# Kernel optimization log

Measured on AMD Instinct MI355X. Metric: run time of the kernel, lower is better.

The kernel has to match this reference:

```python
import jax, jax.numpy as jnp
import numpy as np

B, C, H, W_sp = 32, 64, 64, 64
K, D = 512, 64

def setup_inputs() -> dict:
    key = jax.random.key(0)
    k1, k2 = jax.random.split(key)
    x = jax.random.normal(k1, (B, C, H, W_sp), dtype=jnp.float32)
    # codebook init uniform(-1/K, 1/K) as in the torch module
    W = jax.random.uniform(k2, (K, D), dtype=jnp.float32, minval=-1.0 / K, maxval=1.0 / K)
    return {"x": x, "W": W}

def reference(x, W):
    # NCHW -> NHWC, flatten to [N, D]
    inputs = jnp.transpose(x, (0, 2, 3, 1))  # [B,H,W,D]
    input_shape = inputs.shape
    flat = inputs.reshape(-1, D)  # [N, D]
    # squared euclidean distances [N, K]
    distances = (jnp.sum(flat * flat, axis=1, keepdims=True)
                 + jnp.sum(W * W, axis=1)
                 - 2.0 * jnp.matmul(flat, W.T))
    encoding_indices = jnp.argmin(distances, axis=1)[:, None]  # [N,1]
    encodings = jax.nn.one_hot(encoding_indices[:, 0], K, dtype=jnp.float32)  # [N,K]
    # direct gather instead of one-hot matmul (same math)
    quantized = W[encoding_indices[:, 0]].reshape(input_shape)  # [B,H,W,D]
    # straight-through estimator
    quantized = inputs + jax.lax.stop_gradient(quantized - inputs)
    avg_probs = jnp.mean(encodings, axis=0)  # [K]
    perplexity = jnp.exp(-jnp.sum(avg_probs * jnp.log(avg_probs + 1e-10)))
    quantized = jnp.transpose(quantized, (0, 3, 1, 2))  # back to NCHW
    return (distances, encodings, encoding_indices, quantized, perplexity)
```

## Files before the change

kernel.cpp:

```cpp
#include <hip/hip_runtime.h>
#include <float.h>
#include <math.h>

#define NROWS 131072
#define KCB   512
#define DDIM  64
#define HWSP  4096
#define BCHW  8388608

__global__ __launch_bounds__(256) void vq_main(const float* __restrict__ x,
                                               const float* __restrict__ Wc,
                                               float* __restrict__ dist,
                                               float* __restrict__ enc,
                                               float* __restrict__ idxo) {
    __shared__ float lx[DDIM][64];
    __shared__ float lw[DDIM][68];
    __shared__ float lxsq[64];
    __shared__ float lwsq[64];

    const int t  = threadIdx.x;
    const int n0 = blockIdx.x * 64;
    const int b  = n0 >> 12;
    const int s0 = n0 & (HWSP - 1);

    {
        const int s = t & 63, cq = t >> 6;
        const float* xb = x + (size_t)b * DDIM * HWSP + s0 + s;
#pragma unroll
        for (int it = 0; it < 16; ++it) {
            const int c = it * 4 + cq;
            lx[c][s] = xb[(size_t)c * HWSP];
        }
    }
    __syncthreads();
    if (t < 64) {
        float s = 0.f;
#pragma unroll
        for (int d = 0; d < DDIM; ++d) { const float v = lx[d][t]; s += v * v; }
        lxsq[t] = s;
    }

    const int rg = t >> 4;
    const int kg = t & 15;

    float best[4] = {FLT_MAX, FLT_MAX, FLT_MAX, FLT_MAX};
    int   bidx[4] = {0, 0, 0, 0};

    for (int kt = 0; kt < 8; ++kt) {
        __syncthreads();
        {
            const int d = t & 63, kq0 = t >> 6;
            const float* wb = Wc + (size_t)(kt * 64) * DDIM + d;
#pragma unroll
            for (int it = 0; it < 16; ++it) {
                const int kq = it * 4 + kq0;
                lw[d][kq] = wb[(size_t)kq * DDIM];
            }
        }
        __syncthreads();
        if (t < 64) {
            float s = 0.f;
#pragma unroll
            for (int d = 0; d < DDIM; ++d) { const float w = lw[d][t]; s += w * w; }
            lwsq[t] = s;
        }
        __syncthreads();

        float acc[4][4] = {};
#pragma unroll 4
        for (int d = 0; d < DDIM; ++d) {
            const float4 xv = *(const float4*)&lx[d][rg * 4];
            const float4 wv = *(const float4*)&lw[d][kg * 4];
            acc[0][0] += xv.x * wv.x; acc[0][1] += xv.x * wv.y; acc[0][2] += xv.x * wv.z; acc[0][3] += xv.x * wv.w;
            acc[1][0] += xv.y * wv.x; acc[1][1] += xv.y * wv.y; acc[1][2] += xv.y * wv.z; acc[1][3] += xv.y * wv.w;
            acc[2][0] += xv.z * wv.x; acc[2][1] += xv.z * wv.y; acc[2][2] += xv.z * wv.z; acc[2][3] += xv.z * wv.w;
            acc[3][0] += xv.w * wv.x; acc[3][1] += xv.w * wv.y; acc[3][2] += xv.w * wv.z; acc[3][3] += xv.w * wv.w;
        }

        const int kbase = kt * 64 + kg * 4;
        const float4 wq = *(const float4*)&lwsq[kg * 4];
        const float4 z4 = make_float4(0.f, 0.f, 0.f, 0.f);
#pragma unroll
        for (int r = 0; r < 4; ++r) {
            const int n = n0 + rg * 4 + r;
            const float xs = lxsq[rg * 4 + r];
            float4 dv;
            dv.x = xs + wq.x - 2.f * acc[r][0];
            dv.y = xs + wq.y - 2.f * acc[r][1];
            dv.z = xs + wq.z - 2.f * acc[r][2];
            dv.w = xs + wq.w - 2.f * acc[r][3];
            *(float4*)&dist[(size_t)n * KCB + kbase] = dv;
            *(float4*)&enc [(size_t)n * KCB + kbase] = z4;
            const float dd[4] = {dv.x, dv.y, dv.z, dv.w};
#pragma unroll
            for (int j = 0; j < 4; ++j) {
                const int kk = kbase + j;
                if (dd[j] < best[r] || (dd[j] == best[r] && kk < bidx[r])) {
                    best[r] = dd[j]; bidx[r] = kk;
                }
            }
        }
    }

#pragma unroll
    for (int off = 8; off >= 1; off >>= 1) {
#pragma unroll
        for (int r = 0; r < 4; ++r) {
            const float od = __shfl_xor(best[r], off);
            const int   oi = __shfl_xor(bidx[r], off);
            if (od < best[r] || (od == best[r] && oi < bidx[r])) { best[r] = od; bidx[r] = oi; }
        }
    }

    __syncthreads();
    if (kg == 0) {
#pragma unroll
        for (int r = 0; r < 4; ++r) {
            const int n = n0 + rg * 4 + r;
            idxo[n] = (float)bidx[r];
            enc[(size_t)n * KCB + bidx[r]] = 1.0f;
        }
    }
}

__global__ __launch_bounds__(256) void vq_quant(const float* __restrict__ Wc,
                                                const float* __restrict__ idxf,
                                                float* __restrict__ qout) {
    __shared__ float lq[64][65];
    __shared__ int   codes[64];

    const int t  = threadIdx.x;
    const int n0 = blockIdx.x * 64;
    const int b  = n0 >> 12;
    const int s0 = n0 & (HWSP - 1);

    if (t < 64) codes[t] = (int)idxf[n0 + t];
    __syncthreads();
    {
        const int c = t & 63, rq = t >> 6;
#pragma unroll
        for (int it = 0; it < 16; ++it) {
            const int r = it * 4 + rq;
            lq[r][c] = Wc[(size_t)codes[r] * DDIM + c];
        }
    }
    __syncthreads();
    {
        const int s = t & 63, cq = t >> 6;
        float* qb = qout + (size_t)b * DDIM * HWSP + s0 + s;
#pragma unroll
        for (int it = 0; it < 16; ++it) {
            const int c = it * 4 + cq;
            qb[(size_t)c * HWSP] = lq[s][c];
        }
    }
}

__global__ __launch_bounds__(512) void vq_perp(const float* __restrict__ idxf,
                                               float* __restrict__ perp) {
    __shared__ unsigned int lh[KCB];
    __shared__ float red[8];
    const int t = threadIdx.x;
    lh[t] = 0u;
    __syncthreads();
    for (int i = t; i < NROWS; i += 512)
        atomicAdd(&lh[(int)idxf[i]], 1u);
    __syncthreads();
    const float p = (float)lh[t] * (1.0f / (float)NROWS);
    float term = p * logf(p + 1e-10f);
#pragma unroll
    for (int off = 32; off >= 1; off >>= 1) term += __shfl_down(term, off);
    if ((t & 63) == 0) red[t >> 6] = term;
    __syncthreads();
    if (t == 0) {
        float s = 0.f;
#pragma unroll
        for (int i = 0; i < 8; ++i) s += red[i];
        *perp = expf(-s);
    }
}

extern "C" void kernel_launch(void* const* d_in, const int* in_sizes, int n_in,
                              void* d_out, int out_size, void* d_ws, size_t ws_size,
                              hipStream_t stream) {
    const float* x  = (const float*)d_in[0];
    const float* Wc = (const float*)d_in[1];

    float* out = (float*)d_out;
    const size_t NK = (size_t)NROWS * KCB;
    float* dist  = out;
    float* enc   = out + NK;
    float* idxo  = out + 2 * NK;
    float* quant = idxo + NROWS;
    float* perp  = quant + (size_t)BCHW;

    (void)d_ws; (void)ws_size;

    vq_main <<<NROWS / 64, 256, 0, stream>>>(x, Wc, dist, enc, idxo);
    vq_quant<<<NROWS / 64, 256, 0, stream>>>(Wc, idxo, quant);
    vq_perp <<<1,          512, 0, stream>>>(idxo, perp);
}
```

Baseline: 717.8 us.

## Enlarge distance-GEMM register tile to 8x8 and precompute codebook norms once

The main kernel now processes 128 rows per block against 128-code tiles. Each thread holds an 8x8 accumulator instead of 4x4, which gives more FMAs per shared-memory load and halves the number of codebook reloads per row. All 512 codebook squared norms are computed once per block from global memory rather than per tile, which removes one barrier per tile. The perplexity histogram kernel moves to 1024 threads with float4 index loads. The larger accumulator raises register pressure and may reduce occupancy, while the kernel remains dominated by the large distance and one-hot output writes.

```diff
diff --git a/kernel.cpp b/kernel.cpp
--- a/kernel.cpp
+++ b/kernel.cpp
@@ -8,117 +8,148 @@
 #define HWSP  4096
 #define BCHW  8388608
 
+#define BM    128
+#define BKT   128
+#define NT    4
+
 __global__ __launch_bounds__(256) void vq_main(const float* __restrict__ x,
                                                const float* __restrict__ Wc,
                                                float* __restrict__ dist,
                                                float* __restrict__ enc,
                                                float* __restrict__ idxo) {
-    __shared__ float lx[DDIM][64];
-    __shared__ float lw[DDIM][68];
-    __shared__ float lxsq[64];
-    __shared__ float lwsq[64];
+    __shared__ float lx[DDIM][BM];
+    __shared__ float lw[DDIM][BKT];
+    __shared__ float lxsq[BM];
+    __shared__ float lwsq[KCB];
 
     const int t  = threadIdx.x;
-    const int n0 = blockIdx.x * 64;
+    const int n0 = blockIdx.x * BM;
     const int b  = n0 >> 12;
     const int s0 = n0 & (HWSP - 1);
 
     {
-        const int s = t & 63, cq = t >> 6;
-        const float* xb = x + (size_t)b * DDIM * HWSP + s0 + s;
-#pragma unroll
-        for (int it = 0; it < 16; ++it) {
-            const int c = it * 4 + cq;
+        const int s = t & 127, cq = t >> 7;
+        const float* xb = x + (size_t)b * (DDIM * HWSP) + s0 + s;
+#pragma unroll
+        for (int it = 0; it < 32; ++it) {
+            const int c = it * 2 + cq;
             lx[c][s] = xb[(size_t)c * HWSP];
         }
     }
-    __syncthreads();
-    if (t < 64) {
+    {
+#pragma unroll
+        for (int kk = 0; kk < 2; ++kk) {
+            const int k = t + kk * 256;
+            const float4* wr = (const float4*)(Wc + (size_t)k * DDIM);
+            float s = 0.f;
+#pragma unroll
+            for (int j = 0; j < 16; ++j) {
+                const float4 v = wr[j];
+                s += v.x * v.x + v.y * v.y + v.z * v.z + v.w * v.w;
+            }
+            lwsq[k] = s;
+        }
+    }
+    __syncthreads();
+    if (t < BM) {
         float s = 0.f;
 #pragma unroll
         for (int d = 0; d < DDIM; ++d) { const float v = lx[d][t]; s += v * v; }
         lxsq[t] = s;
     }
 
-    const int rg = t >> 4;
-    const int kg = t & 15;
-
-    float best[4] = {FLT_MAX, FLT_MAX, FLT_MAX, FLT_MAX};
-    int   bidx[4] = {0, 0, 0, 0};
-
-    for (int kt = 0; kt < 8; ++kt) {
+    const int tr = t >> 4;
+    const int tc = t & 15;
+
+    float best[8];
+    int   bidx[8];
+#pragma unroll
+    for (int i = 0; i < 8; ++i) { best[i] = FLT_MAX; bidx[i] = 0; }
+
+    for (int kt = 0; kt < NT; ++kt) {
         __syncthreads();
         {
             const int d = t & 63, kq0 = t >> 6;
-            const float* wb = Wc + (size_t)(kt * 64) * DDIM + d;
-#pragma unroll
-            for (int it = 0; it < 16; ++it) {
+            const float* wb = Wc + (size_t)(kt * BKT) * DDIM + d;
+#pragma unroll
+            for (int it = 0; it < 32; ++it) {
                 const int kq = it * 4 + kq0;
                 lw[d][kq] = wb[(size_t)kq * DDIM];
             }
         }
         __syncthreads();
-        if (t < 64) {
-            float s = 0.f;
-#pragma unroll
-            for (int d = 0; d < DDIM; ++d) { const float w = lw[d][t]; s += w * w; }
-            lwsq[t] = s;
-        }
-        __syncthreads();
-
-        float acc[4][4] = {};
+
+        float acc[8][8] = {};
 #pragma unroll 4
         for (int d = 0; d < DDIM; ++d) {
-            const float4 xv = *(const float4*)&lx[d][rg * 4];
-            const float4 wv = *(const float4*)&lw[d][kg * 4];
-            acc[0][0] += xv.x * wv.x; acc[0][1] += xv.x * wv.y; acc[0][2] += xv.x * wv.z; acc[0][3] += xv.x * wv.w;
-            acc[1][0] += xv.y * wv.x; acc[1][1] += xv.y * wv.y; acc[1][2] += xv.y * wv.z; acc[1][3] += xv.y * wv.w;
-            acc[2][0] += xv.z * wv.x; acc[2][1] += xv.z * wv.y; acc[2][2] += xv.z * wv.z; acc[2][3] += xv.z * wv.w;
-            acc[3][0] += xv.w * wv.x; acc[3][1] += xv.w * wv.y; acc[3][2] += xv.w * wv.z; acc[3][3] += xv.w * wv.w;
-        }
-
-        const int kbase = kt * 64 + kg * 4;
-        const float4 wq = *(const float4*)&lwsq[kg * 4];
+            const float4 xv0 = *(const float4*)&lx[d][tr * 4];
+            const float4 xv1 = *(const float4*)&lx[d][64 + tr * 4];
+            const float4 wv0 = *(const float4*)&lw[d][tc * 4];
+            const float4 wv1 = *(const float4*)&lw[d][64 + tc * 4];
+            const float xv[8] = {xv0.x, xv0.y, xv0.z, xv0.w, xv1.x, xv1.y, xv1.z, xv1.w};
+            const float wv[8] = {wv0.x, wv0.y, wv0.z, wv0.w, wv1.x, wv1.y, wv1.z, wv1.w};
+#pragma unroll
+            for (int i = 0; i < 8; ++i)
+#pragma unroll
+                for (int j = 0; j < 8; ++j)
+                    acc[i][j] += xv[i] * wv[j];
+        }
+
+        const int kb = kt * BKT;
         const float4 z4 = make_float4(0.f, 0.f, 0.f, 0.f);
 #pragma unroll
-        for (int r = 0; r < 4; ++r) {
-            const int n = n0 + rg * 4 + r;
-            const float xs = lxsq[rg * 4 + r];
-            float4 dv;
-            dv.x = xs + wq.x - 2.f * acc[r][0];
-            dv.y = xs + wq.y - 2.f * acc[r][1];
-            dv.z = xs + wq.z - 2.f * acc[r][2];
-            dv.w = xs + wq.w - 2.f * acc[r][3];
-            *(float4*)&dist[(size_t)n * KCB + kbase] = dv;
-            *(float4*)&enc [(size_t)n * KCB + kbase] = z4;
-            const float dd[4] = {dv.x, dv.y, dv.z, dv.w};
-#pragma unroll
-            for (int j = 0; j < 4; ++j) {
-                const int kk = kbase + j;
-                if (dd[j] < best[r] || (dd[j] == best[r] && kk < bidx[r])) {
-                    best[r] = dd[j]; bidx[r] = kk;
+        for (int h = 0; h < 2; ++h)
+#pragma unroll
+        for (int i = 0; i < 4; ++i) {
+            const int r = h * 64 + tr * 4 + i;
+            const int n = n0 + r;
+            const float xs = lxsq[r];
+            float* drow = &dist[(size_t)n * KCB + kb];
+            float* erow = &enc [(size_t)n * KCB + kb];
+#pragma unroll
+            for (int g = 0; g < 2; ++g) {
+                const int kc = g * 64 + tc * 4;
+                const float4 wq = *(const float4*)&lwsq[kb + kc];
+                float4 dv;
+                dv.x = xs + wq.x - 2.f * acc[h * 4 + i][g * 4 + 0];
+                dv.y = xs + wq.y - 2.f * acc[h * 4 + i][g * 4 + 1];
+                dv.z = xs + wq.z - 2.f * acc[h * 4 + i][g * 4 + 2];
+                dv.w = xs + wq.w - 2.f * acc[h * 4 + i][g * 4 + 3];
+                *(float4*)&drow[kc] = dv;
+                *(float4*)&erow[kc] = z4;
+                const float dd[4] = {dv.x, dv.y, dv.z, dv.w};
+#pragma unroll
+                for (int j = 0; j < 4; ++j) {
+                    const int kk = kb + kc + j;
+                    const int a  = h * 4 + i;
+                    if (dd[j] < best[a] || (dd[j] == best[a] && kk < bidx[a])) {
+                        best[a] = dd[j]; bidx[a] = kk;
+                    }
                 }
             }
         }
     }
 
 #pragma unroll
-    for (int off = 8; off >= 1; off >>= 1) {
-#pragma unroll
-        for (int r = 0; r < 4; ++r) {
-            const float od = __shfl_xor(best[r], off);
-            const int   oi = __shfl_xor(bidx[r], off);
-            if (od < best[r] || (od == best[r] && oi < bidx[r])) { best[r] = od; bidx[r] = oi; }
-        }
-    }
-
-    __syncthreads();
-    if (kg == 0) {
-#pragma unroll
-        for (int r = 0; r < 4; ++r) {
-            const int n = n0 + rg * 4 + r;
-            idxo[n] = (float)bidx[r];
-            enc[(size_t)n * KCB + bidx[r]] = 1.0f;
+    for (int off = 8; off >= 1; off >>= 1)
+#pragma unroll
+        for (int i = 0; i < 8; ++i) {
+            const float od = __shfl_xor(best[i], off);
+            const int   oi = __shfl_xor(bidx[i], off);
+            if (od < best[i] || (od == best[i] && oi < bidx[i])) { best[i] = od; bidx[i] = oi; }
+        }
+
+    __syncthreads();
+    if (tc == 0) {
+#pragma unroll
+        for (int h = 0; h < 2; ++h)
+#pragma unroll
+        for (int i = 0; i < 4; ++i) {
+            const int r  = h * 64 + tr * 4 + i;
+            const int n  = n0 + r;
+            const int bi = bidx[h * 4 + i];
+            idxo[n] = (float)bi;
+            enc[(size_t)n * KCB + bi] = 1.0f;
         }
     }
 }
@@ -147,7 +178,7 @@
     __syncthreads();
     {
         const int s = t & 63, cq = t >> 6;
-        float* qb = qout + (size_t)b * DDIM * HWSP + s0 + s;
+        float* qb = qout + (size_t)b * (DDIM * HWSP) + s0 + s;
 #pragma unroll
         for (int it = 0; it < 16; ++it) {
             const int c = it * 4 + cq;
@@ -156,18 +187,29 @@
     }
 }
 
-__global__ __launch_bounds__(512) void vq_perp(const float* __restrict__ idxf,
-                                               float* __restrict__ perp) {
+__global__ __launch_bounds__(1024) void vq_perp(const float* __restrict__ idxf,
+                                                float* __restrict__ perp) {
     __shared__ unsigned int lh[KCB];
-    __shared__ float red[8];
+    __shared__ float red[16];
     const int t = threadIdx.x;
-    lh[t] = 0u;
-    __syncthreads();
-    for (int i = t; i < NROWS; i += 512)
-        atomicAdd(&lh[(int)idxf[i]], 1u);
-    __syncthreads();
-    const float p = (float)lh[t] * (1.0f / (float)NROWS);
-    float term = p * logf(p + 1e-10f);
+    if (t < KCB) lh[t] = 0u;
+    if (t < 16) red[t] = 0.f;
+    __syncthreads();
+    const float4* p4 = (const float4*)idxf;
+#pragma unroll 4
+    for (int j = 0; j < 32; ++j) {
+        const float4 v = p4[t + j * 1024];
+        atomicAdd(&lh[(int)v.x], 1u);
+        atomicAdd(&lh[(int)v.y], 1u);
+        atomicAdd(&lh[(int)v.z], 1u);
+        atomicAdd(&lh[(int)v.w], 1u);
+    }
+    __syncthreads();
+    float term = 0.f;
+    if (t < KCB) {
+        const float p = (float)lh[t] * (1.0f / (float)NROWS);
+        term = p * logf(p + 1e-10f);
+    }
 #pragma unroll
     for (int off = 32; off >= 1; off >>= 1) term += __shfl_down(term, off);
     if ((t & 63) == 0) red[t >> 6] = term;
@@ -175,7 +217,7 @@
     if (t == 0) {
         float s = 0.f;
 #pragma unroll
-        for (int i = 0; i < 8; ++i) s += red[i];
+        for (int i = 0; i < 16; ++i) s += red[i];
         *perp = expf(-s);
     }
 }
@@ -196,7 +238,7 @@
 
     (void)d_ws; (void)ws_size;
 
-    vq_main <<<NROWS / 64, 256, 0, stream>>>(x, Wc, dist, enc, idxo);
-    vq_quant<<<NROWS / 64, 256, 0, stream>>>(Wc, idxo, quant);
-    vq_perp <<<1,          512, 0, stream>>>(idxo, perp);
-}
+    vq_main <<<NROWS / BM, 256,  0, stream>>>(x, Wc, dist, enc, idxo);
+    vq_quant<<<NROWS / 64, 256,  0, stream>>>(Wc, idxo, quant);
+    vq_perp <<<1,          1024, 0, stream>>>(idxo, perp);
+}
```

Result: slower. 736.3 us (+2.6%).
